# Optimization experiments

Hardware: AMD Instinct MI355X
Metric: run time of the kernel (lower is better)

## Reference

```python
import jax, jax.numpy as jnp
import numpy as np

D_MODEL = 512
D_STATE = 16
D_INNER = 2 * D_MODEL  # expand_factor=2
IN_CH = 256
B_SZ, H_SZ, W_SZ = 4, 32, 32


def setup_inputs() -> dict:
    key = jax.random.key(0)
    ks = jax.random.split(key, 24)
    f = jax.random.normal
    inp = {}
    inp["x_V"] = f(ks[0], (B_SZ, IN_CH, H_SZ, W_SZ), jnp.float32)
    inp["x_I"] = f(ks[1], (B_SZ, IN_CH, H_SZ, W_SZ), jnp.float32)
    # channel_reduce: 1x1 conv + BN (inference stats)
    inp["conv_red_w"] = f(ks[2], (D_MODEL, IN_CH), jnp.float32) * 0.05
    inp["bn_red_g"] = jnp.ones((D_MODEL,), jnp.float32)
    inp["bn_red_b"] = jnp.zeros((D_MODEL,), jnp.float32)
    inp["bn_red_m"] = jnp.zeros((D_MODEL,), jnp.float32)
    inp["bn_red_v"] = jnp.ones((D_MODEL,), jnp.float32)
    # channel_restore: 1x1 conv + BN
    inp["conv_res_w"] = f(ks[3], (IN_CH, D_MODEL), jnp.float32) * 0.05
    inp["bn_res_g"] = jnp.ones((IN_CH,), jnp.float32)
    inp["bn_res_b"] = jnp.zeros((IN_CH,), jnp.float32)
    inp["bn_res_m"] = jnp.zeros((IN_CH,), jnp.float32)
    inp["bn_res_v"] = jnp.ones((IN_CH,), jnp.float32)
    # lambda_predictor convs (1x1 on pooled features == linear)
    inp["lam_w1"] = f(ks[4], (D_MODEL // 4, D_MODEL * 2), jnp.float32) * 0.05
    inp["lam_b1"] = jnp.zeros((D_MODEL // 4,), jnp.float32)
    inp["lam_w2"] = f(ks[5], (2, D_MODEL // 4), jnp.float32) * 0.05
    inp["lam_b2"] = jnp.zeros((2,), jnp.float32)
    # two SimplifiedMamba2Blocks
    for i, p in enumerate(["V", "I"]):
        kk = jax.random.split(ks[6 + i], 6)
        inp[p + "_in_w"] = f(kk[0], (2 * D_INNER, D_MODEL), jnp.float32) * 0.03
        inp[p + "_out_w"] = f(kk[1], (D_MODEL, D_INNER), jnp.float32) * 0.03
        # A = -exp(A_log) in (-1, -0.05): stable decay
        inp[p + "_A_log"] = jnp.log(jax.random.uniform(kk[2], (D_INNER, D_STATE), jnp.float32, 0.05, 0.95))
        inp[p + "_B"] = f(kk[3], (D_INNER, D_STATE), jnp.float32) * 0.05
        inp[p + "_C"] = jnp.full((D_INNER, D_STATE), 0.01, jnp.float32)
        inp[p + "_ln_g"] = jnp.ones((D_MODEL,), jnp.float32)
        inp[p + "_ln_b"] = jnp.zeros((D_MODEL,), jnp.float32)
    inp["gate"] = jnp.asarray(0.1, jnp.float32)
    return inp


def _bn(x, g, b, m, v):
    # x: (B,C,H,W); inference-mode batchnorm
    return (x - m[:, None, None]) / jnp.sqrt(v[:, None, None] + 1e-5) * g[:, None, None] + b[:, None, None]


def _conv1x1(x, w):
    return jnp.einsum('bchw,oc->bohw', x, w)


def _ssm_scan(x_ssm, A, Bm, Cm, reverse):
    # x_ssm: (B,L,I); A,Bm,Cm: (I,S)
    bsz = x_ssm.shape[0]
    h0 = jnp.zeros((bsz, A.shape[0], A.shape[1]), x_ssm.dtype)

    def step(h, xt):  # xt: (B,I)
        h = jnp.clip(h * A + xt[:, :, None] * Bm, -10.0, 10.0)
        return h, jnp.einsum('bis,is->bi', h, Cm)

    _, ys = jax.lax.scan(step, h0, jnp.swapaxes(x_ssm, 0, 1), reverse=reverse)
    return jnp.swapaxes(ys, 0, 1)  # (B,L,I), in original time order


def _mamba(x, ln_g, ln_b, in_w, out_w, A_log, Bm, Cm):
    # LayerNorm
    mu = jnp.mean(x, -1, keepdims=True)
    var = jnp.mean((x - mu) ** 2, -1, keepdims=True)
    xn = (x - mu) / jnp.sqrt(var + 1e-5) * ln_g + ln_b
    xp = xn @ in_w.T  # (B,L,2*I)
    x_ssm, gate = jnp.split(xp, 2, axis=-1)
    A = jnp.clip(-jnp.exp(A_log), -10.0, -0.01)
    yf = _ssm_scan(x_ssm, A, Bm, Cm, False)
    yb = _ssm_scan(x_ssm, A, Bm, Cm, True)
    out = 0.5 * (yf + yb) * jax.nn.silu(gate)
    return out @ out_w.T


def reference(x_V, x_I, conv_red_w, bn_red_g, bn_red_b, bn_red_m, bn_red_v,
              conv_res_w, bn_res_g, bn_res_b, bn_res_m, bn_res_v,
              lam_w1, lam_b1, lam_w2, lam_b2,
              V_in_w, V_out_w, V_A_log, V_B, V_C, V_ln_g, V_ln_b,
              I_in_w, I_out_w, I_A_log, I_B, I_C, I_ln_g, I_ln_b, gate):
    B, _, H, W = x_V.shape
    xVr = jax.nn.relu(_bn(_conv1x1(x_V, conv_red_w), bn_red_g, bn_red_b, bn_red_m, bn_red_v))
    xIr = jax.nn.relu(_bn(_conv1x1(x_I, conv_red_w), bn_red_g, bn_red_b, bn_red_m, bn_red_v))
    # same spatial size -> adaptive pooling and [:B] slicing are identities
    conc = jnp.concatenate([xVr, xIr], axis=1)  # (B, 2*d_model, H, W)

    def lam(c):
        p = jnp.mean(c, axis=(2, 3))  # global avg pool -> (B, 2*d_model)
        h1 = jax.nn.relu(p @ lam_w1.T + lam_b1)
        return jax.nn.softmax(h1 @ lam_w2.T + lam_b2, axis=-1)  # (B,2)

    lamV = lam(conc)
    lamI = lam(conc)

    seq_V = jnp.swapaxes(xVr.reshape(B, D_MODEL, H * W), 1, 2)  # (B,L,D)
    seq_I = jnp.swapaxes(xIr.reshape(B, D_MODEL, H * W), 1, 2)

    outV_std = _mamba(seq_V, V_ln_g, V_ln_b, V_in_w, V_out_w, V_A_log, V_B, V_C)
    outI_std = _mamba(seq_I, I_ln_g, I_ln_b, I_in_w, I_out_w, I_A_log, I_B, I_C)
    outV_cross = _mamba(seq_V, V_ln_g, V_ln_b, V_in_w, V_out_w, V_A_log, jax.lax.stop_gradient(I_B), V_C)
    outI_cross = _mamba(seq_I, I_ln_g, I_ln_b, I_in_w, I_out_w, I_A_log, jax.lax.stop_gradient(V_B), I_C)

    outV = lamV[:, 0][:, None, None] * outV_std + lamV[:, 1][:, None, None] * outV_cross
    outI = lamI[:, 0][:, None, None] * outI_std + lamI[:, 1][:, None, None] * outI_cross

    featV = jnp.swapaxes(outV, 1, 2).reshape(B, D_MODEL, H, W)
    featI = jnp.swapaxes(outI, 1, 2).reshape(B, D_MODEL, H, W)
    featV = _bn(_conv1x1(featV, conv_res_w), bn_res_g, bn_res_b, bn_res_m, bn_res_v)
    featI = _bn(_conv1x1(featI, conv_res_w), bn_res_g, bn_res_b, bn_res_m, bn_res_v)

    g = jax.nn.sigmoid(gate)
    return (x_V + g * featV, x_I + g * featI)
```

## Files before the change

kernel.cpp:

```cpp
#include <hip/hip_runtime.h>
#include <hip/hip_bf16.h>
#include <math.h>

#define L_SZ 1024
#define DM   512
#define DI   1024
#define NS   16
#define CH   256

typedef float4 f4;
typedef __attribute__((ext_vector_type(8))) short short8;
typedef __attribute__((ext_vector_type(8))) unsigned short u16x8;
typedef __attribute__((ext_vector_type(4))) float f32x4;

__device__ __forceinline__ float bf2f(ushort u) {
    union { unsigned int i; float f; } x; x.i = ((unsigned int)u) << 16; return x.f;
}
__device__ __forceinline__ ushort f2bf(float f) {
    union { float f; unsigned int i; } x; x.f = f;
    unsigned int r = x.i + 0x7FFFu + ((x.i >> 16) & 1u);
    return (ushort)(r >> 16);
}
__device__ __forceinline__ uint pkbf(float a, float b) {
    union { __hip_bfloat162 h; uint u; } c;
    c.h = __float22bfloat162_rn(make_float2(a, b));
    return c.u;
}

#define GLOAD16(gp, lp) \
  __builtin_amdgcn_global_load_lds((const __attribute__((address_space(1))) void*)(gp), \
                                   (__attribute__((address_space(3))) void*)(lp), 16, 0, 0)

__global__ __launch_bounds__(256) void k_prep(
    const float* __restrict__ s0, const float* __restrict__ s1,
    const float* __restrict__ s2, const float* __restrict__ s3,
    const float* __restrict__ s4, const float* __restrict__ s5,
    ushort* __restrict__ d0, ushort* __restrict__ d1,
    ushort* __restrict__ d2, ushort* __restrict__ d3,
    ushort* __restrict__ d4, ushort* __restrict__ d5,
    const float* __restrict__ xv, const float* __restrict__ xi,
    ushort* __restrict__ xtv, ushort* __restrict__ xti,
    float* __restrict__ p, unsigned int* __restrict__ cnt)
{
    __shared__ float tile[32][36];
    const int bid = blockIdx.x;
    const int t = threadIdx.x;
    if (bid < 3328) {
        const float* s; ushort* d; int rel;
        if      (bid < 128)  { s = s0; d = d0; rel = bid; }
        else if (bid < 256)  { s = s1; d = d1; rel = bid - 128; }
        else if (bid < 1280) { s = s2; d = d2; rel = bid - 256; }
        else if (bid < 2304) { s = s3; d = d3; rel = bid - 1280; }
        else if (bid < 2816) { s = s4; d = d4; rel = bid - 2304; }
        else                 { s = s5; d = d5; rel = bid - 2816; }
        const int i = rel * 256 + t;
        f4 v = ((const f4*)s)[i];
        ushort4 o;
        o.x = f2bf(v.x); o.y = f2bf(v.y); o.z = f2bf(v.z); o.w = f2bf(v.w);
        ((ushort4*)d)[i] = o;
        return;
    }
    if (bid < 5376) {
        const int rel = bid - 3328;
        const int l0 = (rel & 31) * 32, c0 = ((rel >> 5) & 7) * 32;
        const int z = rel >> 8;
        const int b = z & 3, st = z >> 2;
        const float* x = st ? xi : xv;
        ushort* xt = st ? xti : xtv;
        {
            int cc = t >> 3, ll4 = (t & 7) << 2;
            f4 v = *(const f4*)(x + ((size_t)(b * CH + c0 + cc)) * L_SZ + l0 + ll4);
            tile[cc][ll4 + 0] = v.x; tile[cc][ll4 + 1] = v.y;
            tile[cc][ll4 + 2] = v.z; tile[cc][ll4 + 3] = v.w;
        }
        __syncthreads();
        {
            int ll = t >> 3, cc4 = (t & 7) << 2;
            ushort4 o;
            o.x = f2bf(tile[cc4 + 0][ll]); o.y = f2bf(tile[cc4 + 1][ll]);
            o.z = f2bf(tile[cc4 + 2][ll]); o.w = f2bf(tile[cc4 + 3][ll]);
            *(ushort4*)(xt + ((size_t)(b * L_SZ + l0 + ll)) * CH + c0 + cc4) = o;
        }
        return;
    }
    const f4 z4 = {0.f, 0.f, 0.f, 0.f};
    ((f4*)p)[t]       = z4;
    ((f4*)p)[t + 256] = z4;
    ((f4*)p)[t + 512] = z4;
    ((f4*)p)[t + 768] = z4;
    if (t == 0) *cnt = 0u;
}

template<int MODE, int BM, int BN>
__global__ __launch_bounds__(256) void k_gemm(
    const ushort* __restrict__ A0, const ushort* __restrict__ A1,
    const ushort* __restrict__ B0, const ushort* __restrict__ B1,
    int K,
    float* __restrict__ o0, float* __restrict__ o1,
    ushort* __restrict__ ob0, ushort* __restrict__ ob1,
    ushort* __restrict__ sb0, ushort* __restrict__ sb1,
    const float* __restrict__ pg, const float* __restrict__ pb,
    const float* __restrict__ pm, const float* __restrict__ pv,
    const float* __restrict__ x0, const float* __restrict__ x1,
    const float* __restrict__ gate, float* __restrict__ pp)
{
    constexpr int MT   = BM / 32;
    constexpr int NT   = BN / 32;
    constexpr int ASEG = BM / 16;
    constexpr int NSEG = (BM + BN) / 16;
    constexpr int SPW  = NSEG / 4;
    __shared__ __align__(16) ushort Sl[(BM + BN) * 32];
    const int t = threadIdx.x;
    const int wv = t >> 6, lane = t & 63;
    const int n0 = blockIdx.x * BN, m0 = blockIdx.y * BM;
    const int st = blockIdx.z;
    const ushort* Ap = st ? A1 : A0;
    const ushort* Bp = st ? B1 : B0;
    const int wm = wv >> 1, wn = wv & 1;
    const int lrow = lane & 15, q = lane >> 4;
    f32x4 acc[MT][NT];
    #pragma unroll
    for (int a_ = 0; a_ < MT; ++a_)
        #pragma unroll
        for (int b_ = 0; b_ < NT; ++b_)
            acc[a_][b_] = (f32x4){0.f, 0.f, 0.f, 0.f};
    const int srow = lane >> 2;
    const int skk  = (((lane & 3) ^ ((lane >> 3) & 3)) << 3);
    const int koff = ((q ^ ((lrow >> 1) & 3)) << 3);
    for (int k0 = 0; k0 < K; k0 += 32) {
        #pragma unroll
        for (int s2 = 0; s2 < SPW; ++s2) {
            const int seg = wv * SPW + s2;
            const int grow = (seg < ASEG) ? (m0 + seg * 16 + srow)
                                          : (n0 + (seg - ASEG) * 16 + srow);
            const ushort* src = (seg < ASEG) ? Ap : Bp;
            GLOAD16(src + (size_t)grow * K + k0 + skk, &Sl[seg * 512]);
        }
        __syncthreads();
        short8 af[MT], bfr[NT];
        #pragma unroll
        for (int mt = 0; mt < MT; ++mt)
            af[mt] = *(const short8*)&Sl[(wm * (MT * 16) + mt * 16 + lrow) * 32 + koff];
        #pragma unroll
        for (int nt = 0; nt < NT; ++nt)
            bfr[nt] = *(const short8*)&Sl[(BM + wn * (NT * 16) + nt * 16 + lrow) * 32 + koff];
        #pragma unroll
        for (int mt = 0; mt < MT; ++mt)
            #pragma unroll
            for (int nt = 0; nt < NT; ++nt)
                acc[mt][nt] = __builtin_amdgcn_mfma_f32_16x16x32_bf16(af[mt], bfr[nt], acc[mt][nt], 0, 0, 0);
        __syncthreads();
    }
    if (MODE == 0) {
        ushort* sq = st ? ob1 : ob0;
        const int b = m0 >> 10;
        #pragma unroll
        for (int nt = 0; nt < NT; ++nt) {
            const int gn = n0 + wn * (NT * 16) + nt * 16 + lrow;
            const float s  = pg[gn] * rsqrtf(pv[gn] + 1e-5f);
            const float sh = pb[gn] - pm[gn] * s;
            float psum = 0.f;
            #pragma unroll
            for (int mt = 0; mt < MT; ++mt) {
                const int gm = m0 + wm * (MT * 16) + mt * 16 + q * 4;
                float v[4];
                #pragma unroll
                for (int r = 0; r < 4; ++r) {
                    v[r] = fmaxf(fmaf(acc[mt][nt][r], s, sh), 0.f);
                    psum += v[r];
                }
                const uint u01 = pkbf(v[0], v[1]);
                const uint u23 = pkbf(v[2], v[3]);
                ushort* bp = sq + (size_t)gm * DM + gn;
                bp[0]      = (ushort)u01;
                bp[DM]     = (ushort)(u01 >> 16);
                bp[2 * DM] = (ushort)u23;
                bp[3 * DM] = (ushort)(u23 >> 16);
            }
            psum += __shfl_xor(psum, 16, 64);
            psum += __shfl_xor(psum, 32, 64);
            if (q == 0)
                atomicAdd(pp + (b * 1024 + st * 512 + gn), psum * (1.0f / 1024.0f));
        }
    } else if (MODE == 1) {
        const bool isx = (n0 < 1024);
        ushort* xp = st ? ob1 : ob0;
        ushort* sp = st ? sb1 : sb0;
        #pragma unroll
        for (int nt = 0; nt < NT; ++nt) {
            const int gn = n0 + wn * (NT * 16) + nt * 16 + lrow;
            #pragma unroll
            for (int mt = 0; mt < MT; ++mt) {
                const int gm = m0 + wm * (MT * 16) + mt * 16 + q * 4;
                if (isx) {
                    const uint u01 = pkbf(acc[mt][nt][0], acc[mt][nt][1]);
                    const uint u23 = pkbf(acc[mt][nt][2], acc[mt][nt][3]);
                    ushort* bp = xp + (size_t)gm * DI + gn;
                    bp[0]      = (ushort)u01;
                    bp[DI]     = (ushort)(u01 >> 16);
                    bp[2 * DI] = (ushort)u23;
                    bp[3 * DI] = (ushort)(u23 >> 16);
                } else {
                    float sv[4];
                    #pragma unroll
                    for (int r = 0; r < 4; ++r) {
                        const float v = acc[mt][nt][r];
                        sv[r] = v / (1.f + __expf(-v));
                    }
                    const uint u01 = pkbf(sv[0], sv[1]);
                    const uint u23 = pkbf(sv[2], sv[3]);
                    ushort* bp = sp + (size_t)gm * DI + gn - 1024;
                    bp[0]      = (ushort)u01;
                    bp[DI]     = (ushort)(u01 >> 16);
                    bp[2 * DI] = (ushort)u23;
                    bp[3 * DI] = (ushort)(u23 >> 16);
                }
            }
        }
    } else if (MODE == 2) {
        ushort* fp_ = st ? ob1 : ob0;
        #pragma unroll
        for (int nt = 0; nt < NT; ++nt) {
            const int gn = n0 + wn * (NT * 16) + nt * 16 + lrow;
            #pragma unroll
            for (int mt = 0; mt < MT; ++mt) {
                const int gm = m0 + wm * (MT * 16) + mt * 16 + q * 4;
                const uint u01 = pkbf(acc[mt][nt][0], acc[mt][nt][1]);
                const uint u23 = pkbf(acc[mt][nt][2], acc[mt][nt][3]);
                ushort* bp = fp_ + (size_t)gm * DM + gn;
                bp[0]      = (ushort)u01;
                bp[DM]     = (ushort)(u01 >> 16);
                bp[2 * DM] = (ushort)u23;
                bp[3 * DM] = (ushort)(u23 >> 16);
            }
        }
    } else {
        const float* xin = st ? x1 : x0;
        float* op = st ? o1 : o0;
        const float g = 1.f / (1.f + __expf(-gate[0]));
        #pragma unroll
        for (int nt = 0; nt < NT; ++nt) {
            const int gn = n0 + wn * (NT * 16) + nt * 16 + lrow;
            const float s  = pg[gn] * rsqrtf(pv[gn] + 1e-5f);
            const float sh = pb[gn] - pm[gn] * s;
            #pragma unroll
            for (int mt = 0; mt < MT; ++mt) {
                const int gmb = m0 + wm * (MT * 16) + mt * 16 + q * 4;
                const int b = gmb >> 10, l = gmb & 1023;
                const size_t off = ((size_t)(b * CH + gn)) * L_SZ + l;
                f4 xi = *(const f4*)(xin + off);
                f4 o;
                o.x = xi.x + g * fmaf(acc[mt][nt][0], s, sh);
                o.y = xi.y + g * fmaf(acc[mt][nt][1], s, sh);
                o.z = xi.z + g * fmaf(acc[mt][nt][2], s, sh);
                o.w = xi.w + g * fmaf(acc[mt][nt][3], s, sh);
                *(f4*)(op + off) = o;
            }
        }
    }
}

__global__ __launch_bounds__(256) void k_lam(
    const float* __restrict__ p, const float* __restrict__ w1,
    const float* __restrict__ b1, const float* __restrict__ w2,
    const float* __restrict__ b2, float* __restrict__ h1,
    float* __restrict__ lam, unsigned int* __restrict__ cnt)
{
    __shared__ float lsm[8];
    __shared__ unsigned int tick;
    const int t = threadIdx.x, lane = t & 63, wv = t >> 6;
    const int idx = blockIdx.x * 4 + wv;
    const int b = idx >> 7, j = idx & 127;
    const float* pb = p + b * 1024;
    const float* wr = w1 + j * 1024;
    float s = 0.f;
    #pragma unroll
    for (int k = 0; k < 16; ++k)
        s = fmaf(pb[lane + k * 64], wr[lane + k * 64], s);
    #pragma unroll
    for (int off = 1; off < 64; off <<= 1) s += __shfl_xor(s, off, 64);
    if (lane == 0) h1[idx] = fmaxf(s + b1[j], 0.f);
    __threadfence();
    __syncthreads();
    if (t == 0) tick = atomicAdd(cnt, 1u);
    __syncthreads();
    if (tick != 127u) return;
    __threadfence();
    {
        const int g32 = t >> 5, l32 = t & 31;
        const int bb = g32 >> 1, kk = g32 & 1;
        const float* hb = h1 + bb * 128;
        const float* wr2 = w2 + kk * 128;
        float ss = 0.f;
        #pragma unroll
        for (int u = 0; u < 4; ++u)
            ss = fmaf(hb[l32 + u * 32], wr2[l32 + u * 32], ss);
        #pragma unroll
        for (int off = 1; off < 32; off <<= 1) ss += __shfl_xor(ss, off, 64);
        if (l32 == 0) lsm[g32] = ss + b2[kk];
    }
    __syncthreads();
    if (t < 4) {
        const float a0 = lsm[t * 2], a1 = lsm[t * 2 + 1];
        const float m  = fmaxf(a0, a1);
        const float e0 = __expf(a0 - m), e1 = __expf(a1 - m);
        const float inv = 1.f / (e0 + e1);
        lam[t * 2 + 0] = e0 * inv;
        lam[t * 2 + 1] = e1 * inv;
    }
}

__global__ __launch_bounds__(256) void k_ln(
    const ushort* __restrict__ seq0, const ushort* __restrict__ seq1,
    const float* __restrict__ g0, const float* __restrict__ b0,
    const float* __restrict__ g1, const float* __restrict__ b1,
    ushort* __restrict__ ln0, ushort* __restrict__ ln1)
{
    const int t = threadIdx.x, lane = t & 63, wv = t >> 6;
    const int row = blockIdx.x * 4 + wv, st = blockIdx.y;
    const ushort* seq = st ? seq1 : seq0;
    const float* gg  = st ? g1 : g0;
    const float* bb  = st ? b1 : b0;
    ushort* ln = st ? ln1 : ln0;
    const u16x8 v = *(const u16x8*)(seq + (size_t)row * DM + lane * 8);
    float f[8];
    float s = 0.f, ss = 0.f;
    #pragma unroll
    for (int i = 0; i < 8; ++i) {
        f[i] = bf2f(v[i]);
        s += f[i];
        ss = fmaf(f[i], f[i], ss);
    }
    #pragma unroll
    for (int off = 1; off < 64; off <<= 1) {
        s += __shfl_xor(s, off, 64); ss += __shfl_xor(ss, off, 64);
    }
    const float mu = s * (1.f / 512.f);
    const float rstd = rsqrtf(ss * (1.f / 512.f) - mu * mu + 1e-5f);
    const f4 gv0 = *(const f4*)(gg + lane * 8);
    const f4 gv1 = *(const f4*)(gg + lane * 8 + 4);
    const f4 bv0 = *(const f4*)(bb + lane * 8);
    const f4 bv1 = *(const f4*)(bb + lane * 8 + 4);
    const float gvv[8] = {gv0.x, gv0.y, gv0.z, gv0.w, gv1.x, gv1.y, gv1.z, gv1.w};
    const float bvv[8] = {bv0.x, bv0.y, bv0.z, bv0.w, bv1.x, bv1.y, bv1.z, bv1.w};
    u16x8 o;
    #pragma unroll
    for (int i = 0; i < 8; i += 2) {
        const uint u = pkbf(fmaf((f[i]     - mu) * rstd, gvv[i],     bvv[i]),
                            fmaf((f[i + 1] - mu) * rstd, gvv[i + 1], bvv[i + 1]));
        o[i]     = (ushort)u;
        o[i + 1] = (ushort)(u >> 16);
    }
    *(u16x8*)(ln + (size_t)row * DM + lane * 8) = o;
}

__global__ __launch_bounds__(256) void k_scan(
    const ushort* __restrict__ xsV, const ushort* __restrict__ xsI,
    const ushort* __restrict__ sgV, const ushort* __restrict__ sgI,
    const float* __restrict__ VA, const float* __restrict__ VB,
    const float* __restrict__ VC, const float* __restrict__ IA,
    const float* __restrict__ IB, const float* __restrict__ IC,
    const float* __restrict__ lam,
    ushort* __restrict__ yV, ushort* __restrict__ yI)
{
    __shared__ __align__(16) ushort xf[2][16][128];
    __shared__ __align__(16) ushort xb[2][16][128];
    __shared__ ushort yfb[32][128];
    __shared__ ushort ybb[32][128];
    const int t = threadIdx.x;
    const int shalf = t & 1;
    const int il = t >> 1;
    const int b = blockIdx.y;
    const int st = blockIdx.z >> 4, j = blockIdx.z & 15;
    const ushort* xrow  = (st ? xsI : xsV) + (size_t)b * L_SZ * DI + blockIdx.x * 128;
    const ushort* sgrow = (st ? sgI : sgV) + (size_t)b * L_SZ * DI + blockIdx.x * 128;
    ushort* yrow        = (st ? yI  : yV ) + (size_t)b * L_SZ * DI + blockIdx.x * 128;
    const float* Alog = st ? IA : VA;
    const float* Cm   = st ? IC : VC;
    const float* Bown = st ? IB : VB;
    const float* Both = st ? VB : IB;
    const float lam0 = lam[b * 2 + 0], lam1 = lam[b * 2 + 1];
    float a[8], w[8], gf[8], gb[8];
    const int base = (blockIdx.x * 128 + il) * NS + shalf * 8;
    #pragma unroll
    for (int s = 0; s < 8; ++s) {
        a[s] = fminf(fmaxf(-__expf(Alog[base + s]), -10.f), -0.01f);
        w[s] = 0.5f * Cm[base + s] * fmaf(lam0, Bown[base + s], lam1 * Both[base + s]);
        gf[s] = 0.f; gb[s] = 0.f;
    }
    const int row0 = j << 6;
    const int srow = t >> 4;
    const int scol = (t & 15) << 3;
    {
        int rf = row0 - 64 + srow;          rf = max(0, min(1023, rf));
        GLOAD16(xrow + (size_t)rf * DI + scol, &xf[0][srow][0]);
        int rb = row0 + 127 - srow;         rb = max(0, min(1023, rb));
        GLOAD16(xrow + (size_t)rb * DI + scol, &xb[0][srow][0]);
    }
    __syncthreads();
    for (int si = 0; si < 8; ++si) {
        const int buf = si & 1;
        if (si < 7) {
            const int base2 = (si + 1) * 16;
            int rf = row0 - 64 + base2 + srow;  rf = max(0, min(1023, rf));
            GLOAD16(xrow + (size_t)rf * DI + scol, &xf[buf ^ 1][srow][0]);
            int rb = row0 + 127 - base2 - srow; rb = max(0, min(1023, rb));
            GLOAD16(xrow + (size_t)rb * DI + scol, &xb[buf ^ 1][srow][0]);
        }
        if (si == 4) {
            if (j == 0) {
                for (int s = 0; s < 8; ++s) gf[s] = 0.f;
            }
            if (j == 15) {
                for (int s = 0; s < 8; ++s) gb[s] = 0.f;
            }
        }
        if (si < 4) {
            #pragma unroll
            for (int n = 0; n < 16; ++n) {
                const float vf = bf2f(xf[buf][n][il]);
                const float vb = bf2f(xb[buf][n][il]);
                #pragma unroll
                for (int s = 0; s < 8; ++s) {
                    gf[s] = fmaf(a[s], gf[s], vf);
                    gb[s] = fmaf(a[s], gb[s], vb);
                }
            }
        } else if (si < 6) {
            const int mb = (si - 4) * 16;
            #pragma unroll
            for (int n = 0; n < 16; ++n) {
                const float vf = bf2f(xf[buf][n][il]);
                const float vb = bf2f(xb[buf][n][il]);
                float yf = 0.f, yb = 0.f;
                #pragma unroll
                for (int s = 0; s < 8; ++s) {
                    gf[s] = fmaf(a[s], gf[s], vf);
                    yf    = fmaf(gf[s], w[s], yf);
                    gb[s] = fmaf(a[s], gb[s], vb);
                    yb    = fmaf(gb[s], w[s], yb);
                }
                yf += __shfl_xor(yf, 1, 64);
                yb += __shfl_xor(yb, 1, 64);
                if (shalf == 0) {
                    const int m = mb + n;
                    yfb[m][il]      = f2bf(yf);
                    ybb[31 - m][il] = f2bf(yb);
                }
            }
        } else {
            const int mb = (si - 6) * 16 + 32;
            #pragma unroll
            for (int n = 0; n < 16; ++n) {
                const float vf = bf2f(xf[buf][n][il]);
                const float vb = bf2f(xb[buf][n][il]);
                float yf = 0.f, yb = 0.f;
                #pragma unroll
                for (int s = 0; s < 8; ++s) {
                    gf[s] = fmaf(a[s], gf[s], vf);
                    yf    = fmaf(gf[s], w[s], yf);
                    gb[s] = fmaf(a[s], gb[s], vb);
                    yb    = fmaf(gb[s], w[s], yb);
                }
                yf += __shfl_xor(yf, 1, 64);
                yb += __shfl_xor(yb, 1, 64);
                if (shalf == 0) {
                    const int m = mb + n;
                    const int rF = row0 + m;
                    const float zf = (yf + bf2f(ybb[m - 32][il]))
                                   * bf2f(sgrow[(size_t)rF * DI + il]);
                    yrow[(size_t)rF * DI + il] = f2bf(zf);
                    const int rB = row0 + 63 - m;
                    const float zb = (yb + bf2f(yfb[63 - m][il]))
                                   * bf2f(sgrow[(size_t)rB * DI + il]);
                    yrow[(size_t)rB * DI + il] = f2bf(zb);
                }
            }
        }
        __syncthreads();
    }
}

extern "C" void kernel_launch(void* const* d_in, const int* in_sizes, int n_in,
                              void* d_out, int out_size, void* d_ws, size_t ws_size,
                              hipStream_t stream)
{
    const float* xV       = (const float*)d_in[0];
    const float* xI       = (const float*)d_in[1];
    const float* convredw = (const float*)d_in[2];
    const float* bnredg   = (const float*)d_in[3];
    const float* bnredb   = (const float*)d_in[4];
    const float* bnredm   = (const float*)d_in[5];
    const float* bnredv   = (const float*)d_in[6];
    const float* convresw = (const float*)d_in[7];
    const float* bnresg   = (const float*)d_in[8];
    const float* bnresb   = (const float*)d_in[9];
    const float* bnresm   = (const float*)d_in[10];
    const float* bnresv   = (const float*)d_in[11];
    const float* lamw1    = (const float*)d_in[12];
    const float* lamb1    = (const float*)d_in[13];
    const float* lamw2    = (const float*)d_in[14];
    const float* lamb2    = (const float*)d_in[15];
    const float* Vinw     = (const float*)d_in[16];
    const float* Voutw    = (const float*)d_in[17];
    const float* VAlog    = (const float*)d_in[18];
    const float* VB       = (const float*)d_in[19];
    const float* VC       = (const float*)d_in[20];
    const float* Vlng     = (const float*)d_in[21];
    const float* Vlnb     = (const float*)d_in[22];
    const float* Iinw     = (const float*)d_in[23];
    const float* Ioutw    = (const float*)d_in[24];
    const float* IAlog    = (const float*)d_in[25];
    const float* IB       = (const float*)d_in[26];
    const float* IC       = (const float*)d_in[27];
    const float* Ilng     = (const float*)d_in[28];
    const float* Ilnb     = (const float*)d_in[29];
    const float* gate     = (const float*)d_in[30];

    char* W = (char*)d_ws;
    const size_t MB = 1048576;
    ushort* seqV  = (ushort*)(W + 0);
    ushort* seqI  = (ushort*)(W + 4  * MB);
    float*  p     = (float*)(W + 8 * MB);
    float*  lam   = (float*)(W + 8 * MB + 16384);
    float*  h1    = (float*)(W + 8 * MB + 32768);
    unsigned int* cnt = (unsigned int*)(W + 8 * MB + 49152);
    ushort* sgV   = (ushort*)(W + 17 * MB);
    ushort* sgI   = (ushort*)(W + 25 * MB);
    ushort* yV    = (ushort*)(W + 33 * MB);
    ushort* yI    = (ushort*)(W + 41 * MB);
    ushort* wred  = (ushort*)(W + 65 * MB);
    ushort* wres  = (ushort*)(W + 65 * MB + 262144);
    ushort* winV  = (ushort*)(W + 66 * MB);
    ushort* winI  = (ushort*)(W + 68 * MB);
    ushort* woutV = (ushort*)(W + 70 * MB);
    ushort* woutI = (ushort*)(W + 71 * MB);
    ushort* xtV   = (ushort*)(W + 72 * MB);
    ushort* xtI   = (ushort*)(W + 74 * MB);
    ushort* lnV   = (ushort*)(W + 76 * MB);
    ushort* lnI   = (ushort*)(W + 80 * MB);
    ushort* xsV   = (ushort*)(W + 84 * MB);
    ushort* xsI   = (ushort*)(W + 92 * MB);
    ushort* featV = seqV;
    ushort* featI = seqI;
    float*  outp  = (float*)d_out;

    k_prep<<<dim3(5377), 256, 0, stream>>>(
        convredw, convresw, Vinw, Iinw, Voutw, Ioutw,
        wred, wres, winV, winI, woutV, woutI,
        xV, xI, xtV, xtI, p, cnt);
    k_gemm<0, 128, 64><<<dim3(8, 32, 2), 256, 0, stream>>>(xtV, xtI, wred, wred, 256,
        nullptr, nullptr, seqV, seqI, nullptr, nullptr,
        bnredg, bnredb, bnredm, bnredv, nullptr, nullptr, nullptr, p);
    k_lam<<<128, 256, 0, stream>>>(p, lamw1, lamb1, lamw2, lamb2, h1, lam, cnt);
    k_ln<<<dim3(1024, 2), 256, 0, stream>>>(seqV, seqI, Vlng, Vlnb, Ilng, Ilnb, lnV, lnI);
    k_gemm<1, 128, 128><<<dim3(16, 32, 2), 256, 0, stream>>>(lnV, lnI, winV, winI, 512,
        nullptr, nullptr, xsV, xsI, sgV, sgI,
        nullptr, nullptr, nullptr, nullptr, nullptr, nullptr, nullptr, nullptr);
    k_scan<<<dim3(8, 4, 32), 256, 0, stream>>>(xsV, xsI, sgV, sgI,
        VAlog, VB, VC, IAlog, IB, IC, lam, yV, yI);
    k_gemm<2, 128, 64><<<dim3(8, 32, 2), 256, 0, stream>>>(yV, yI, woutV, woutI, 1024,
        nullptr, nullptr, featV, featI, nullptr, nullptr,
        nullptr, nullptr, nullptr, nullptr, nullptr, nullptr, nullptr, nullptr);
    k_gemm<3, 64, 64><<<dim3(4, 64, 2), 256, 0, stream>>>(featV, featI, wres, wres, 512,
        outp, outp + 1048576, nullptr, nullptr, nullptr, nullptr,
        bnresg, bnresb, bnresm, bnresv, xV, xI, gate, nullptr);
}
```

Before: 260.8 us.

## Fold LayerNorm into in-projection GEMM via row stats and weight prescaling

```diff
diff --git a/kernel.cpp b/kernel.cpp
--- a/kernel.cpp
+++ b/kernel.cpp
@@ -40,21 +40,30 @@
     ushort* __restrict__ d4, ushort* __restrict__ d5,
     const float* __restrict__ xv, const float* __restrict__ xi,
     ushort* __restrict__ xtv, ushort* __restrict__ xti,
+    const float* __restrict__ vg, const float* __restrict__ ig,
+    const float* __restrict__ vb, const float* __restrict__ ib,
+    float* __restrict__ sgw, float* __restrict__ bz2,
     float* __restrict__ p, unsigned int* __restrict__ cnt)
 {
     __shared__ float tile[32][36];
     const int bid = blockIdx.x;
     const int t = threadIdx.x;
+    const int lane = t & 63, wv = t >> 6;
     if (bid < 3328) {
-        const float* s; ushort* d; int rel;
+        const float* s; ushort* d; int rel; int scale = 0; const float* g = nullptr;
         if      (bid < 128)  { s = s0; d = d0; rel = bid; }
         else if (bid < 256)  { s = s1; d = d1; rel = bid - 128; }
-        else if (bid < 1280) { s = s2; d = d2; rel = bid - 256; }
-        else if (bid < 2304) { s = s3; d = d3; rel = bid - 1280; }
+        else if (bid < 1280) { s = s2; d = d2; rel = bid - 256;  scale = 1; g = vg; }
+        else if (bid < 2304) { s = s3; d = d3; rel = bid - 1280; scale = 1; g = ig; }
         else if (bid < 2816) { s = s4; d = d4; rel = bid - 2304; }
         else                 { s = s5; d = d5; rel = bid - 2816; }
         const int i = rel * 256 + t;
         f4 v = ((const f4*)s)[i];
+        if (scale) {
+            const int k4 = (i * 4) & 511;
+            f4 gv = *(const f4*)(g + k4);
+            v.x *= gv.x; v.y *= gv.y; v.z *= gv.z; v.w *= gv.w;
+        }
         ushort4 o;
         o.x = f2bf(v.x); o.y = f2bf(v.y); o.z = f2bf(v.z); o.w = f2bf(v.w);
         ((ushort4*)d)[i] = o;
@@ -83,11 +92,33 @@
         }
         return;
     }
+    if (bid < 6400) {
+        const int idx = (bid - 5376) * 4 + wv;
+        const int st = idx >> 11, j = idx & 2047;
+        const float* wrow = (st ? s3 : s2) + (size_t)j * 512;
+        const float* gv = st ? ig : vg;
+        const float* bv = st ? ib : vb;
+        float sw = 0.f, bz = 0.f;
+        #pragma unroll
+        for (int u = 0; u < 8; ++u) {
+            const int k = lane + u * 64;
+            const float wk = wrow[k];
+            sw = fmaf(wk, gv[k], sw);
+            bz = fmaf(wk, bv[k], bz);
+        }
+        #pragma unroll
+        for (int off = 1; off < 64; off <<= 1) {
+            sw += __shfl_xor(sw, off, 64);
+            bz += __shfl_xor(bz, off, 64);
+        }
+        if (lane == 0) {
+            sgw[st * 2048 + j] = sw;
+            bz2[st * 2048 + j] = bz;
+        }
+        return;
+    }
     const f4 z4 = {0.f, 0.f, 0.f, 0.f};
-    ((f4*)p)[t]       = z4;
-    ((f4*)p)[t + 256] = z4;
-    ((f4*)p)[t + 512] = z4;
-    ((f4*)p)[t + 768] = z4;
+    for (int i = t; i < 5120; i += 256) ((f4*)p)[i] = z4;
     if (t == 0) *cnt = 0u;
 }
 
@@ -102,7 +133,8 @@
     const float* __restrict__ pg, const float* __restrict__ pb,
     const float* __restrict__ pm, const float* __restrict__ pv,
     const float* __restrict__ x0, const float* __restrict__ x1,
-    const float* __restrict__ gate, float* __restrict__ pp)
+    const float* __restrict__ gate, float* __restrict__ pp,
+    float* __restrict__ q0, float* __restrict__ q1)
 {
     constexpr int MT   = BM / 32;
     constexpr int NT   = BN / 32;
@@ -153,7 +185,11 @@
     }
     if (MODE == 0) {
         ushort* sq = st ? ob1 : ob0;
+        float* ss = st ? q1 : q0;
         const int b = m0 >> 10;
+        float rs[MT * 4], rq[MT * 4];
+        #pragma unroll
+        for (int i = 0; i < MT * 4; ++i) { rs[i] = 0.f; rq[i] = 0.f; }
         #pragma unroll
         for (int nt = 0; nt < NT; ++nt) {
             const int gn = n0 + wn * (NT * 16) + nt * 16 + lrow;
@@ -168,6 +204,8 @@
                 for (int r = 0; r < 4; ++r) {
                     v[r] = fmaxf(fmaf(acc[mt][nt][r], s, sh), 0.f);
                     psum += v[r];
+                    rs[mt * 4 + r] += v[r];
+                    rq[mt * 4 + r] = fmaf(v[r], v[r], rq[mt * 4 + r]);
                 }
                 const uint u01 = pkbf(v[0], v[1]);
                 const uint u23 = pkbf(v[2], v[3]);
@@ -182,33 +220,72 @@
             if (q == 0)
                 atomicAdd(pp + (b * 1024 + st * 512 + gn), psum * (1.0f / 1024.0f));
         }
+        #pragma unroll
+        for (int i = 0; i < MT * 4; ++i) {
+            float s1 = rs[i], s2 = rq[i];
+            #pragma unroll
+            for (int off = 1; off < 16; off <<= 1) {
+                s1 += __shfl_xor(s1, off, 64);
+                s2 += __shfl_xor(s2, off, 64);
+            }
+            rs[i] = s1; rq[i] = s2;
+        }
+        if (lrow == 0) {
+            #pragma unroll
+            for (int mt = 0; mt < MT; ++mt) {
+                const int gm = m0 + wm * (MT * 16) + mt * 16 + q * 4;
+                #pragma unroll
+                for (int r = 0; r < 4; ++r) {
+                    atomicAdd(ss + gm + r, rs[mt * 4 + r]);
+                    atomicAdd(ss + 4096 + gm + r, rq[mt * 4 + r]);
+                }
+            }
+        }
     } else if (MODE == 1) {
+        const float* ss = st ? pb : pg;
+        const float* sw = pm + st * 2048;
+        const float* bz = pv + st * 2048;
+        float mus[MT * 4], rss[MT * 4];
+        #pragma unroll
+        for (int mt = 0; mt < MT; ++mt)
+            #pragma unroll
+            for (int r = 0; r < 4; ++r) {
+                const int row = m0 + wm * (MT * 16) + mt * 16 + q * 4 + r;
+                const float mu = ss[row] * (1.f / 512.f);
+                const float var = ss[4096 + row] * (1.f / 512.f) - mu * mu;
+                mus[mt * 4 + r] = mu;
+                rss[mt * 4 + r] = rsqrtf(var + 1e-5f);
+            }
         const bool isx = (n0 < 1024);
         ushort* xp = st ? ob1 : ob0;
         ushort* sp = st ? sb1 : sb0;
         #pragma unroll
         for (int nt = 0; nt < NT; ++nt) {
             const int gn = n0 + wn * (NT * 16) + nt * 16 + lrow;
+            const float swn = sw[gn];
+            const float bzn = bz[gn];
             #pragma unroll
             for (int mt = 0; mt < MT; ++mt) {
                 const int gm = m0 + wm * (MT * 16) + mt * 16 + q * 4;
+                float vv[4];
+                #pragma unroll
+                for (int r = 0; r < 4; ++r)
+                    vv[r] = fmaf(rss[mt * 4 + r],
+                                 acc[mt][nt][r] - mus[mt * 4 + r] * swn, bzn);
                 if (isx) {
-                    const uint u01 = pkbf(acc[mt][nt][0], acc[mt][nt][1]);
-                    const uint u23 = pkbf(acc[mt][nt][2], acc[mt][nt][3]);
+                    const uint u01 = pkbf(vv[0], vv[1]);
+                    const uint u23 = pkbf(vv[2], vv[3]);
                     ushort* bp = xp + (size_t)gm * DI + gn;
                     bp[0]      = (ushort)u01;
                     bp[DI]     = (ushort)(u01 >> 16);
                     bp[2 * DI] = (ushort)u23;
                     bp[3 * DI] = (ushort)(u23 >> 16);
                 } else {
-                    float sv[4];
                     #pragma unroll
-                    for (int r = 0; r < 4; ++r) {
-                        const float v = acc[mt][nt][r];
-                        sv[r] = v / (1.f + __expf(-v));
-                    }
-                    const uint u01 = pkbf(sv[0], sv[1]);
-                    const uint u23 = pkbf(sv[2], sv[3]);
+                    for (int r = 0; r < 4; ++r)
+                        vv[r] = vv[r] / (1.f + __expf(-vv[r]));
+                    const uint u01 = pkbf(vv[0], vv[1]);
+                    const uint u23 = pkbf(vv[2], vv[3]);
                     ushort* bp = sp + (size_t)gm * DI + gn - 1024;
                     bp[0]      = (ushort)u01;
                     bp[DI]     = (ushort)(u01 >> 16);
@@ -308,50 +385,6 @@
         lam[t * 2 + 0] = e0 * inv;
         lam[t * 2 + 1] = e1 * inv;
     }
-}
-
-__global__ __launch_bounds__(256) void k_ln(
-    const ushort* __restrict__ seq0, const ushort* __restrict__ seq1,
-    const float* __restrict__ g0, const float* __restrict__ b0,
-    const float* __restrict__ g1, const float* __restrict__ b1,
-    ushort* __restrict__ ln0, ushort* __restrict__ ln1)
-{
-    const int t = threadIdx.x, lane = t & 63, wv = t >> 6;
-    const int row = blockIdx.x * 4 + wv, st = blockIdx.y;
-    const ushort* seq = st ? seq1 : seq0;
-    const float* gg  = st ? g1 : g0;
-    const float* bb  = st ? b1 : b0;
-    ushort* ln = st ? ln1 : ln0;
-    const u16x8 v = *(const u16x8*)(seq + (size_t)row * DM + lane * 8);
-    float f[8];
-    float s = 0.f, ss = 0.f;
-    #pragma unroll
-    for (int i = 0; i < 8; ++i) {
-        f[i] = bf2f(v[i]);
-        s += f[i];
-        ss = fmaf(f[i], f[i], ss);
-    }
-    #pragma unroll
-    for (int off = 1; off < 64; off <<= 1) {
-        s += __shfl_xor(s, off, 64); ss += __shfl_xor(ss, off, 64);
-    }
-    const float mu = s * (1.f / 512.f);
-    const float rstd = rsqrtf(ss * (1.f / 512.f) - mu * mu + 1e-5f);
-    const f4 gv0 = *(const f4*)(gg + lane * 8);
-    const f4 gv1 = *(const f4*)(gg + lane * 8 + 4);
-    const f4 bv0 = *(const f4*)(bb + lane * 8);
-    const f4 bv1 = *(const f4*)(bb + lane * 8 + 4);
-    const float gvv[8] = {gv0.x, gv0.y, gv0.z, gv0.w, gv1.x, gv1.y, gv1.z, gv1.w};
-    const float bvv[8] = {bv0.x, bv0.y, bv0.z, bv0.w, bv1.x, bv1.y, bv1.z, bv1.w};
-    u16x8 o;
-    #pragma unroll
-    for (int i = 0; i < 8; i += 2) {
-        const uint u = pkbf(fmaf((f[i]     - mu) * rstd, gvv[i],     bvv[i]),
-                            fmaf((f[i + 1] - mu) * rstd, gvv[i + 1], bvv[i + 1]));
-        o[i]     = (ushort)u;
-        o[i + 1] = (ushort)(u >> 16);
-    }
-    *(u16x8*)(ln + (size_t)row * DM + lane * 8) = o;
 }
 
 __global__ __launch_bounds__(256) void k_scan(
@@ -522,9 +555,13 @@
     ushort* seqV  = (ushort*)(W + 0);
     ushort* seqI  = (ushort*)(W + 4  * MB);
     float*  p     = (float*)(W + 8 * MB);
-    float*  lam   = (float*)(W + 8 * MB + 16384);
-    float*  h1    = (float*)(W + 8 * MB + 32768);
-    unsigned int* cnt = (unsigned int*)(W + 8 * MB + 49152);
+    float*  statsV = (float*)(W + 8 * MB + 16384);
+    float*  statsI = (float*)(W + 8 * MB + 49152);
+    float*  sgWb  = (float*)(W + 8 * MB + 81920);
+    float*  bz2b  = (float*)(W + 8 * MB + 98304);
+    float*  lam   = (float*)(W + 8 * MB + 114688);
+    float*  h1    = (float*)(W + 8 * MB + 118784);
+    unsigned int* cnt = (unsigned int*)(W + 8 * MB + 122880);
     ushort* sgV   = (ushort*)(W + 17 * MB);
     ushort* sgI   = (ushort*)(W + 25 * MB);
     ushort* yV    = (ushort*)(W + 33 * MB);
@@ -537,32 +574,34 @@
     ushort* woutI = (ushort*)(W + 71 * MB);
     ushort* xtV   = (ushort*)(W + 72 * MB);
     ushort* xtI   = (ushort*)(W + 74 * MB);
-    ushort* lnV   = (ushort*)(W + 76 * MB);
-    ushort* lnI   = (ushort*)(W + 80 * MB);
     ushort* xsV   = (ushort*)(W + 84 * MB);
     ushort* xsI   = (ushort*)(W + 92 * MB);
     ushort* featV = seqV;
     ushort* featI = seqI;
     float*  outp  = (float*)d_out;
 
-    k_prep<<<dim3(5377), 256, 0, stream>>>(
+    k_prep<<<dim3(6401), 256, 0, stream>>>(
         convredw, convresw, Vinw, Iinw, Voutw, Ioutw,
         wred, wres, winV, winI, woutV, woutI,
-        xV, xI, xtV, xtI, p, cnt);
+        xV, xI, xtV, xtI,
+        Vlng, Ilng, Vlnb, Ilnb, sgWb, bz2b, p, cnt);
     k_gemm<0, 128, 64><<<dim3(8, 32, 2), 256, 0, stream>>>(xtV, xtI, wred, wred, 256,
         nullptr, nullptr, seqV, seqI, nullptr, nullptr,
-        bnredg, bnredb, bnredm, bnredv, nullptr, nullptr, nullptr, p);
+        bnredg, bnredb, bnredm, bnredv, nullptr, nullptr, nullptr, p,
+        statsV, statsI);
     k_lam<<<128, 256, 0, stream>>>(p, lamw1, lamb1, lamw2, lamb2, h1, lam, cnt);
-    k_ln<<<dim3(1024, 2), 256, 0, stream>>>(seqV, seqI, Vlng, Vlnb, Ilng, Ilnb, lnV, lnI);
-    k_gemm<1, 128, 128><<<dim3(16, 32, 2), 256, 0, stream>>>(lnV, lnI, winV, winI, 512,
+    k_gemm<1, 128, 128><<<dim3(16, 32, 2), 256, 0, stream>>>(seqV, seqI, winV, winI, 512,
         nullptr, nullptr, xsV, xsI, sgV, sgI,
-        nullptr, nullptr, nullptr, nullptr, nullptr, nullptr, nullptr, nullptr);
+        statsV, statsI, sgWb, bz2b, nullptr, nullptr, nullptr, nullptr,
+        nullptr, nullptr);
     k_scan<<<dim3(8, 4, 32), 256, 0, stream>>>(xsV, xsI, sgV, sgI,
         VAlog, VB, VC, IAlog, IB, IC, lam, yV, yI);
     k_gemm<2, 128, 64><<<dim3(8, 32, 2), 256, 0, stream>>>(yV, yI, woutV, woutI, 1024,
         nullptr, nullptr, featV, featI, nullptr, nullptr,
-        nullptr, nullptr, nullptr, nullptr, nullptr, nullptr, nullptr, nullptr);
+        nullptr, nullptr, nullptr, nullptr, nullptr, nullptr, nullptr, nullptr,
+        nullptr, nullptr);
     k_gemm<3, 64, 64><<<dim3(4, 64, 2), 256, 0, stream>>>(featV, featI, wres, wres, 512,
         outp, outp + 1048576, nullptr, nullptr, nullptr, nullptr,
-        bnresg, bnresb, bnresm, bnresv, xV, xI, gate, nullptr);
-}
+        bnresg, bnresb, bnresm, bnresv, xV, xI, gate, nullptr,
+        nullptr, nullptr);
+}
```

After: 269.6 us. 1.03x slower.

## Fold out-projection and channel-restore weights into one combined matrix

Applied to the files above, without the earlier changes.

```diff
diff --git a/kernel.cpp b/kernel.cpp
--- a/kernel.cpp
+++ b/kernel.cpp
@@ -45,19 +45,39 @@
     __shared__ float tile[32][36];
     const int bid = blockIdx.x;
     const int t = threadIdx.x;
-    if (bid < 3328) {
+    if (bid < 2304) {
         const float* s; ushort* d; int rel;
         if      (bid < 128)  { s = s0; d = d0; rel = bid; }
         else if (bid < 256)  { s = s1; d = d1; rel = bid - 128; }
         else if (bid < 1280) { s = s2; d = d2; rel = bid - 256; }
-        else if (bid < 2304) { s = s3; d = d3; rel = bid - 1280; }
-        else if (bid < 2816) { s = s4; d = d4; rel = bid - 2304; }
-        else                 { s = s5; d = d5; rel = bid - 2816; }
+        else                 { s = s3; d = d3; rel = bid - 1280; }
         const int i = rel * 256 + t;
         f4 v = ((const f4*)s)[i];
         ushort4 o;
         o.x = f2bf(v.x); o.y = f2bf(v.y); o.z = f2bf(v.z); o.w = f2bf(v.w);
         ((ushort4*)d)[i] = o;
+        return;
+    }
+    if (bid < 3328) {
+        const int rel = (bid < 2816) ? bid - 2304 : bid - 2816;
+        const float* wo = (bid < 2816) ? s4 : s5;
+        ushort* wt      = (bid < 2816) ? d4 : d5;
+        const int kt = rel & 31, dt = rel >> 5;
+        const int d0_ = dt * 32, k0 = kt * 32;
+        {
+            int cc = t >> 3, ll4 = (t & 7) << 2;
+            f4 v = *(const f4*)(wo + (size_t)(d0_ + cc) * 1024 + k0 + ll4);
+            tile[cc][ll4 + 0] = v.x; tile[cc][ll4 + 1] = v.y;
+            tile[cc][ll4 + 2] = v.z; tile[cc][ll4 + 3] = v.w;
+        }
+        __syncthreads();
+        {
+            int ll = t >> 3, cc4 = (t & 7) << 2;
+            ushort4 o;
+            o.x = f2bf(tile[cc4 + 0][ll]); o.y = f2bf(tile[cc4 + 1][ll]);
+            o.z = f2bf(tile[cc4 + 2][ll]); o.w = f2bf(tile[cc4 + 3][ll]);
+            *(ushort4*)(wt + (size_t)(k0 + ll) * 512 + d0_ + cc4) = o;
+        }
         return;
     }
     if (bid < 5376) {
@@ -91,7 +111,7 @@
     if (t == 0) *cnt = 0u;
 }
 
-template<int MODE, int BM, int BN>
+template<int MODE, int BM, int BN, int OS>
 __global__ __launch_bounds__(256) void k_gemm(
     const ushort* __restrict__ A0, const ushort* __restrict__ A1,
     const ushort* __restrict__ B0, const ushort* __restrict__ B1,
@@ -227,11 +247,11 @@
                 const int gm = m0 + wm * (MT * 16) + mt * 16 + q * 4;
                 const uint u01 = pkbf(acc[mt][nt][0], acc[mt][nt][1]);
                 const uint u23 = pkbf(acc[mt][nt][2], acc[mt][nt][3]);
-                ushort* bp = fp_ + (size_t)gm * DM + gn;
+                ushort* bp = fp_ + (size_t)gm * OS + gn;
                 bp[0]      = (ushort)u01;
-                bp[DM]     = (ushort)(u01 >> 16);
-                bp[2 * DM] = (ushort)u23;
-                bp[3 * DM] = (ushort)(u23 >> 16);
+                bp[OS]     = (ushort)(u01 >> 16);
+                bp[2 * OS] = (ushort)u23;
+                bp[3 * OS] = (ushort)(u23 >> 16);
             }
         }
     } else {
@@ -533,36 +553,37 @@
     ushort* wres  = (ushort*)(W + 65 * MB + 262144);
     ushort* winV  = (ushort*)(W + 66 * MB);
     ushort* winI  = (ushort*)(W + 68 * MB);
-    ushort* woutV = (ushort*)(W + 70 * MB);
-    ushort* woutI = (ushort*)(W + 71 * MB);
+    ushort* woTv  = (ushort*)(W + 70 * MB);
+    ushort* woTi  = (ushort*)(W + 71 * MB);
     ushort* xtV   = (ushort*)(W + 72 * MB);
     ushort* xtI   = (ushort*)(W + 74 * MB);
     ushort* lnV   = (ushort*)(W + 76 * MB);
     ushort* lnI   = (ushort*)(W + 80 * MB);
     ushort* xsV   = (ushort*)(W + 84 * MB);
     ushort* xsI   = (ushort*)(W + 92 * MB);
-    ushort* featV = seqV;
-    ushort* featI = seqI;
+    ushort* wcombV = (ushort*)(W + 100 * MB);
+    ushort* wcombI = (ushort*)(W + 100 * MB + 524288);
     float*  outp  = (float*)d_out;
 
     k_prep<<<dim3(5377), 256, 0, stream>>>(
         convredw, convresw, Vinw, Iinw, Voutw, Ioutw,
-        wred, wres, winV, winI, woutV, woutI,
+        wred, wres, winV, winI, woTv, woTi,
         xV, xI, xtV, xtI, p, cnt);
-    k_gemm<0, 128, 64><<<dim3(8, 32, 2), 256, 0, stream>>>(xtV, xtI, wred, wred, 256,
+    k_gemm<2, 64, 64, 1024><<<dim3(16, 4, 2), 256, 0, stream>>>(
+        wres, wres, woTv, woTi, 512,
+        nullptr, nullptr, wcombV, wcombI, nullptr, nullptr,
+        nullptr, nullptr, nullptr, nullptr, nullptr, nullptr, nullptr, nullptr);
+    k_gemm<0, 128, 64, 512><<<dim3(8, 32, 2), 256, 0, stream>>>(xtV, xtI, wred, wred, 256,
         nullptr, nullptr, seqV, seqI, nullptr, nullptr,
         bnredg, bnredb, bnredm, bnredv, nullptr, nullptr, nullptr, p);
     k_lam<<<128, 256, 0, stream>>>(p, lamw1, lamb1, lamw2, lamb2, h1, lam, cnt);
     k_ln<<<dim3(1024, 2), 256, 0, stream>>>(seqV, seqI, Vlng, Vlnb, Ilng, Ilnb, lnV, lnI);
-    k_gemm<1, 128, 128><<<dim3(16, 32, 2), 256, 0, stream>>>(lnV, lnI, winV, winI, 512,
+    k_gemm<1, 128, 128, 512><<<dim3(16, 32, 2), 256, 0, stream>>>(lnV, lnI, winV, winI, 512,
         nullptr, nullptr, xsV, xsI, sgV, sgI,
         nullptr, nullptr, nullptr, nullptr, nullptr, nullptr, nullptr, nullptr);
     k_scan<<<dim3(8, 4, 32), 256, 0, stream>>>(xsV, xsI, sgV, sgI,
         VAlog, VB, VC, IAlog, IB, IC, lam, yV, yI);
-    k_gemm<2, 128, 64><<<dim3(8, 32, 2), 256, 0, stream>>>(yV, yI, woutV, woutI, 1024,
-        nullptr, nullptr, featV, featI, nullptr, nullptr,
-        nullptr, nullptr, nullptr, nullptr, nullptr, nullptr, nullptr, nullptr);
-    k_gemm<3, 64, 64><<<dim3(4, 64, 2), 256, 0, stream>>>(featV, featI, wres, wres, 512,
+    k_gemm<3, 64, 64, 512><<<dim3(4, 64, 2), 256, 0, stream>>>(yV, yI, wcombV, wcombI, 1024,
         outp, outp + 1048576, nullptr, nullptr, nullptr, nullptr,
         bnresg, bnresb, bnresm, bnresv, xV, xI, gate, nullptr);
 }
```

Measured after the change: 253.3 us. 2.9% less time.
